# Kernel optimization log

Hardware: AMD Instinct MI355X
Metric: run time of the kernel (lower is better)

Reference implementation:

```python
import jax, jax.numpy as jnp
import numpy as np

B, T, S, O = 8, 60, 36, 1
H, E, PE = 4, 16, 16
AD, TA, OUT, L = 12, 10, 64, 2
PRUNE_KEEP_FROM = int(np.floor(S * S * 0.5))  # floor(S^2 * (1 - prune_rate))
EPS = 1e-5


def lrelu(v):
    return jax.nn.leaky_relu(v, 0.01)


def pos_encode(times):
    # standard sinusoidal PE on raw timestamps -> (B, T, PE)
    half = PE // 2
    div = jnp.exp(jnp.arange(half, dtype=jnp.float32) * (-jnp.log(10000.0) / half))
    ang = times[..., None] * div
    return jnp.stack([jnp.sin(ang), jnp.cos(ang)], axis=-1).reshape(times.shape + (PE,))


def pair_sim(adj):
    # sum_{i<j} ||a_i - a_j||^2 = B*sum_i||a_i||^2 - ||sum_i a_i||^2
    b = adj.shape[0]
    sq = jnp.sum(adj * adj)
    tot = jnp.sum(adj, axis=0)
    return (b * sq - jnp.sum(tot * tot)) / ((b - 1) ** 2) / (S * S)


def _forward(x, times, mask, bn_g, bn_b, obs_emb_w, attn_w, bidir_w, proj_W, proj_b,
             Wq, bq, Wk, bk, Ws, bs, lnt_g, lnt_b, Wse, bse, lns_g, lns_b):
    b = x.shape[0]
    # BatchNorm2d over timestep channels (training-mode batch stats)
    mu = x.mean(axis=(0, 2, 3), keepdims=True)
    var = x.var(axis=(0, 2, 3), keepdims=True)
    x = (x - mu) / jnp.sqrt(var + EPS) * bn_g[None, :, None, None] + bn_b[None, :, None, None]
    # per-sensor observation embedding: (B,T,S,O) x (S,O,E*H) -> (B,H,T,S,E)
    h = lrelu(jnp.einsum('btso,som->btsm', x, obs_emb_w))
    h = h.reshape(b, T, S, H, E).transpose(0, 3, 1, 2, 4)
    h = h * mask[:, None, :, :, None]
    pe = pos_encode(times)  # (B,T,PE)
    adj = jnp.ones((b, H, S, S), x.dtype)
    sim = pair_sim(adj)  # 0 for all-ones init, kept for faithfulness
    prune_msk = None
    for lay in range(L):
        hp = h @ proj_W.T + proj_b  # (B,H,T,S,AD+PE)
        cat = jnp.concatenate([
            jnp.broadcast_to(attn_w[lay][None, :, None], (b, H, T, S, AD)),
            jnp.broadcast_to(pe[:, None, :, None], (b, H, T, S, PE))], axis=-1)
        alpha = lrelu(jnp.einsum('bhtsd,bhtjd->bhtsj', hp, cat))  # (B,H,T,S,S)
        if lay:
            cnt = mask.sum(axis=1)[:, None, :, None]  # (B,1,S,1)
            adj = lrelu(adj * (alpha.sum(axis=2) / cnt))
            if prune_msk is None:
                flat = adj.reshape(b, H, S * S)
                ranks = jnp.argsort(jnp.argsort(flat, axis=-1), axis=-1)
                prune_msk = (ranks >= PRUNE_KEEP_FROM).astype(adj.dtype).reshape(b, H, S, S)
            adj = adj * prune_msk
            sim = sim + pair_sim(adj)
        bidir = lrelu(jnp.einsum('hsd,hjd->hsj', bidir_w[lay], bidir_w[lay]))  # (H,S,S)
        w = lrelu(bidir[None, :, None] * alpha * adj[:, :, None])  # (B,H,T,S,S)
        # broadcast message passing: (B,H,T,1,S,E) * (B,H,T,S,S,1) -> sum over source sensor
        h = lrelu(jnp.sum(lrelu(h[:, :, :, None, :, :] * w[..., None]), axis=4))
    pe_e = jnp.broadcast_to(pe[:, None, :, None], (b, H, T, S, PE))
    Hc = jnp.concatenate([h, pe_e], axis=-1).transpose(0, 1, 3, 2, 4)  # (B,H,S,T,E+PE)
    Q = Hc @ Wq.T + bq
    K = Hc @ Wk.T + bk
    beta = jnp.einsum('bhstd,bhsud->bhstu', Q, K)  # (B,H,S,T,T)
    beta = (beta @ Ws.T + bs)[..., 0]  # (B,H,S,T)
    m = beta.mean(axis=(-2, -1), keepdims=True)
    v = beta.var(axis=(-2, -1), keepdims=True)
    beta = (beta - m) / jnp.sqrt(v + EPS) * lnt_g + lnt_b
    out = lrelu(jnp.einsum('bhst,bhstd->bhsd', beta, Hc))
    out = lrelu(out @ Wse.T + bse)
    m2 = out.mean(axis=(-2, -1), keepdims=True)
    v2 = out.var(axis=(-2, -1), keepdims=True)
    out = (out - m2) / jnp.sqrt(v2 + EPS) * lns_g + lns_b
    out = out.transpose(0, 2, 1, 3).reshape(b, S, OUT)
    return out, sim


def setup_inputs():
    key = jax.random.key(0)
    ks = jax.random.split(key, 12)
    def rn(k, shape, scale=0.1):
        return jax.random.normal(k, shape, jnp.float32) * scale
    return {
        'x': jax.random.normal(ks[0], (B, T, S, O), jnp.float32),
        'times': jnp.tile(jnp.arange(T, dtype=jnp.float32), (B, 1)),
        'mask': jnp.ones((B, T, S), jnp.float32),
        'bn_g': jnp.ones((T,), jnp.float32),
        'bn_b': jnp.zeros((T,), jnp.float32),
        'obs_emb_w': rn(ks[1], (S, O, E * H)),
        'attn_w': rn(ks[2], (L, H, S, AD)),
        'bidir_w': rn(ks[3], (L, H, S, AD)),
        'proj_W': rn(ks[4], (AD + PE, E)),
        'proj_b': jnp.zeros((AD + PE,), jnp.float32),
        'Wq': rn(ks[5], (TA, E + PE)),
        'bq': jnp.zeros((TA,), jnp.float32),
        'Wk': rn(ks[6], (TA, E + PE)),
        'bk': jnp.zeros((TA,), jnp.float32),
        'Ws': rn(ks[7], (1, T)),
        'bs': jnp.zeros((1,), jnp.float32),
        'lnt_g': jnp.ones((S, T), jnp.float32),
        'lnt_b': jnp.zeros((S, T), jnp.float32),
        'Wse': rn(ks[8], (OUT // H, E + PE)),
        'bse': jnp.zeros((OUT // H,), jnp.float32),
        'lns_g': jnp.ones((S, OUT // H), jnp.float32),
        'lns_b': jnp.zeros((S, OUT // H), jnp.float32),
    }


def reference(x, times, mask, bn_g, bn_b, obs_emb_w, attn_w, bidir_w, proj_W, proj_b,
              Wq, bq, Wk, bk, Ws, bs, lnt_g, lnt_b, Wse, bse, lns_g, lns_b):
    return _forward(x, times, mask, bn_g, bn_b, obs_emb_w, attn_w, bidir_w, proj_W, proj_b,
                    Wq, bq, Wk, bk, Ws, bs, lnt_g, lnt_b, Wse, bse, lns_g, lns_b)
```

## Files before the change

kernel.cpp:

```cpp
#include <hip/hip_runtime.h>
#include <math.h>

#define Bc 8
#define Tc 60
#define Sc 36
#define Hc_ 4
#define Ec 16
#define PEc 16
#define ADc 12
#define TAc 10
#define OUTc 64
#define KEEP 648
#define EPSc 1e-5f
#define LOG1E4_8 1.15129254649702284f

#define WS_H2     18176
#define WS_H1     1124096
#define WS_ALPHA  2230016
#define WS_ADJ    4759808
#define WS_ADJP   4801280
#define WS_CNT    5050112
#define WS_PE     5050496
#define WS_BETA   WS_ALPHA
#define WS_PART   (WS_ALPHA + 69120)
#define WS_OUT2   (WS_ALPHA + 71424)
#define WS_PART2  (WS_ALPHA + 89856)

__device__ __forceinline__ float lrelu(float v){ return fmaxf(v, 0.01f*v); }

__global__ __launch_bounds__(256) void k_layer01(const float* __restrict__ x,
                          const float* __restrict__ times,
                          const float* __restrict__ mask,
                          const float* __restrict__ bn_g,
                          const float* __restrict__ bn_b,
                          const float* __restrict__ obs_w,
                          const float* __restrict__ attn,
                          const float* __restrict__ bidw,
                          const float* __restrict__ projW,
                          const float* __restrict__ projb,
                          float* __restrict__ ws){
    int idx = blockIdx.x;
    int t = idx % Tc; int bh = idx / Tc; int h = bh % Hc_; int b = bh / Hc_;
    int tid = threadIdx.x;
    __shared__ float sh_h[Sc*Ec];
    __shared__ float sh_h1[Sc*Ec];
    __shared__ float sh_pe[PEc];
    __shared__ float sh_at0T[ADc*Sc];
    __shared__ float sh_at1T[ADc*Sc];
    __shared__ float sh_bwT[ADc*Sc];
    __shared__ float sh_hp[Sc*28];
    __shared__ float sh_P[Sc];
    __shared__ float sh_w[Sc*Sc];
    __shared__ float sh_xn[Sc];
    __shared__ float sh_m[Sc];
    __shared__ float sred[8];
    float s0 = 0.f, s1 = 0.f;
    for (int i = tid; i < Bc*Sc; i += 256){
        float v = x[((i/Sc)*Tc + t)*Sc + (i%Sc)];
        s0 += v; s1 += v*v;
    }
    #pragma unroll
    for (int off = 32; off; off >>= 1){
        s0 += __shfl_down(s0, off, 64);
        s1 += __shfl_down(s1, off, 64);
    }
    if ((tid & 63) == 0){ sred[(tid>>6)*2] = s0; sred[(tid>>6)*2 + 1] = s1; }
    if (tid >= 64 && tid < 80){
        int q = tid - 64; int j = q >> 1;
        float ang = times[b*Tc + t] * expf(-(float)j * LOG1E4_8);
        float pv = (q & 1) ? cosf(ang) : sinf(ang);
        sh_pe[q] = pv;
        if (h == 0) ws[WS_PE + (b*Tc + t)*PEc + q] = pv;
    }
    for (int i = tid; i < ADc*Sc; i += 256){
        int d = i / Sc, j = i % Sc;
        sh_at0T[i] = attn[h*Sc*ADc + j*ADc + d];
        sh_at1T[i] = attn[(Hc_ + h)*Sc*ADc + j*ADc + d];
        sh_bwT[i]  = bidw[h*Sc*ADc + j*ADc + d];
    }
    __syncthreads();
    float mu  = (sred[0]+sred[2]+sred[4]+sred[6]) / (float)(Bc*Sc);
    float var = (sred[1]+sred[3]+sred[5]+sred[7]) / (float)(Bc*Sc) - mu*mu;
    if (tid < Sc){
        float xv = x[(b*Tc + t)*Sc + tid];
        sh_xn[tid] = (xv - mu) * rsqrtf(var + EPSc) * bn_g[t] + bn_b[t];
        sh_m[tid]  = mask[(b*Tc + t)*Sc + tid];
    }
    __syncthreads();
    for (int i = tid; i < Sc*Ec; i += 256){
        int s = i / Ec, e = i % Ec;
        sh_h[i] = lrelu(sh_xn[s]*obs_w[s*64 + h*Ec + e]) * sh_m[s];
    }
    __syncthreads();
    for (int i = tid; i < Sc*28; i += 256){
        int s = i / 28, d = i % 28;
        float acc = projb[d];
        const float* w = projW + d*Ec;
        const float* hh = sh_h + s*Ec;
        #pragma unroll
        for (int e = 0; e < Ec; e++) acc += hh[e]*w[e];
        sh_hp[i] = acc;
    }
    __syncthreads();
    if (tid < Sc){
        const float* hp = sh_hp + tid*28 + ADc;
        float p = 0.f;
        #pragma unroll
        for (int d = 0; d < PEc; d++) p += hp[d]*sh_pe[d];
        sh_P[tid] = p;
    }
    __syncthreads();
    for (int i = tid; i < Sc*Sc; i += 256){
        int s = i / Sc, j = i % Sc;
        const float* hp = sh_hp + s*28;
        float acc = sh_P[s];
        float bd = 0.f;
        #pragma unroll
        for (int d = 0; d < ADc; d++){
            acc += hp[d]*sh_at0T[d*Sc + j];
            bd  += sh_bwT[d*Sc + s]*sh_bwT[d*Sc + j];
        }
        sh_w[i] = lrelu(lrelu(bd)*lrelu(acc));
    }
    __syncthreads();
    float* h1g = ws + WS_H1 + (size_t)idx*Sc*Ec;
    for (int i = tid; i < Sc*Ec; i += 256){
        int s = i / Ec, e = i % Ec;
        float acc = 0.f;
        #pragma unroll 6
        for (int j = 0; j < Sc; j++) acc += lrelu(sh_h[j*Ec + e]*sh_w[s*Sc + j]);
        float v = lrelu(acc);
        sh_h1[i] = v;
        h1g[i] = v;
    }
    __syncthreads();
    for (int i = tid; i < Sc*28; i += 256){
        int s = i / 28, d = i % 28;
        float acc = projb[d];
        const float* w = projW + d*Ec;
        const float* hh = sh_h1 + s*Ec;
        #pragma unroll
        for (int e = 0; e < Ec; e++) acc += hh[e]*w[e];
        sh_hp[i] = acc;
    }
    __syncthreads();
    if (tid < Sc){
        const float* hp = sh_hp + tid*28 + ADc;
        float p = 0.f;
        #pragma unroll
        for (int d = 0; d < PEc; d++) p += hp[d]*sh_pe[d];
        sh_P[tid] = p;
    }
    __syncthreads();
    float* adst = ws + WS_ALPHA + (size_t)idx*Sc*Sc;
    for (int i = tid; i < Sc*Sc; i += 256){
        int s = i / Sc, j = i % Sc;
        const float* hp = sh_hp + s*28;
        float acc = sh_P[s];
        #pragma unroll
        for (int d = 0; d < ADc; d++) acc += hp[d]*sh_at1T[d*Sc + j];
        adst[i] = lrelu(acc);
    }
}

__global__ __launch_bounds__(256) void k_adjpart(const float* __restrict__ mask, float* __restrict__ ws){
    int bh = blockIdx.x / 6; int chunk = blockIdx.x % 6;
    int tid = threadIdx.x;
    const float4* a = (const float4*)(ws + WS_ALPHA + (size_t)bh*Tc*Sc*Sc) + (size_t)chunk*10*324;
    float4* p = (float4*)(ws + WS_ADJP + (size_t)blockIdx.x*Sc*Sc);
    for (int c = tid; c < 324; c += 256){
        float4 acc = make_float4(0.f, 0.f, 0.f, 0.f);
        #pragma unroll
        for (int tt = 0; tt < 10; tt++){
            float4 u = a[(size_t)tt*324 + c];
            acc.x += u.x; acc.y += u.y; acc.z += u.z; acc.w += u.w;
        }
        p[c] = acc;
    }
    if (chunk == 0 && (bh & 3) == 0 && tid < Sc){
        int b = bh >> 2;
        float c = 0.f;
        #pragma unroll 4
        for (int t = 0; t < Tc; t++) c += mask[(b*Tc + t)*Sc + tid];
        ws[WS_CNT + b*Sc + tid] = c;
    }
}

__global__ __launch_bounds__(256) void k_prune(float* __restrict__ ws){
    int bh = blockIdx.x / 24; int chunk = blockIdx.x % 24;
    int b = bh >> 2;
    int tid = threadIdx.x;
    __shared__ __align__(16) float sh_v[Sc*Sc];
    __shared__ float sh_cnt[Sc];
    const float4* p = (const float4*)(ws + WS_ADJP + (size_t)bh*6*Sc*Sc);
    for (int c = tid; c < 324; c += 256){
        float4 acc = make_float4(0.f, 0.f, 0.f, 0.f);
        #pragma unroll
        for (int q = 0; q < 6; q++){
            float4 u = p[(size_t)q*324 + c];
            acc.x += u.x; acc.y += u.y; acc.z += u.z; acc.w += u.w;
        }
        ((float4*)sh_v)[c] = acc;
    }
    if (tid < Sc) sh_cnt[tid] = ws[WS_CNT + b*Sc + tid];
    __syncthreads();
    for (int i = tid; i < Sc*Sc; i += 256){
        int s = i / Sc;
        sh_v[i] = lrelu(sh_v[i] / sh_cnt[s]);
    }
    __syncthreads();
    int r = tid >> 2; if (r > 53) r = 53;
    int part = tid & 3;
    int i = chunk*54 + r;
    float v = sh_v[i];
    const float4* v4 = (const float4*)sh_v + part*81;
    int a0 = part*324;
    int cnt = 0;
    #pragma unroll 9
    for (int j = 0; j < 81; j++){
        float4 u = v4[j];
        int k = a0 + j*4;
        cnt += (int)(u.x < v) + ((int)(u.x == v) & (int)(k   < i));
        cnt += (int)(u.y < v) + ((int)(u.y == v) & (int)(k+1 < i));
        cnt += (int)(u.z < v) + ((int)(u.z == v) & (int)(k+2 < i));
        cnt += (int)(u.w < v) + ((int)(u.w == v) & (int)(k+3 < i));
    }
    cnt += __shfl_down(cnt, 2, 4);
    cnt += __shfl_down(cnt, 1, 4);
    if (part == 0 && tid < 216)
        ws[WS_ADJ + bh*Sc*Sc + i] = (cnt >= KEEP) ? v : 0.f;
}

__global__ __launch_bounds__(256) void k_layer1mp(const float* __restrict__ bidw,
                                                  float* __restrict__ ws){
    int idx = blockIdx.x;
    int t = idx % Tc; int bh = idx / Tc; int h = bh % Hc_;
    int tid = threadIdx.x;
    __shared__ float sh_h[Sc*Ec];
    __shared__ float sh_w[Sc*Sc];
    __shared__ float sh_bwT[ADc*Sc];
    const float* hsrc = ws + WS_H1 + (size_t)idx*Sc*Ec;
    const float* al  = ws + WS_ALPHA + (size_t)idx*Sc*Sc;
    const float* adj = ws + WS_ADJ + bh*Sc*Sc;
    for (int i = tid; i < Sc*Ec; i += 256) sh_h[i] = hsrc[i];
    for (int i = tid; i < ADc*Sc; i += 256){
        int d = i / Sc, j = i % Sc;
        sh_bwT[i] = bidw[(Hc_ + h)*Sc*ADc + j*ADc + d];
    }
    __syncthreads();
    for (int i = tid; i < Sc*Sc; i += 256){
        int s = i / Sc, j = i % Sc;
        float bd = 0.f;
        #pragma unroll
        for (int d = 0; d < ADc; d++) bd += sh_bwT[d*Sc + s]*sh_bwT[d*Sc + j];
        sh_w[i] = lrelu(lrelu(bd)*al[i]*adj[i]);
    }
    __syncthreads();
    for (int i = tid; i < Sc*Ec; i += 256){
        int s = i / Ec, e = i % Ec;
        float acc = 0.f;
        #pragma unroll 6
        for (int j = 0; j < Sc; j++) acc += lrelu(sh_h[j*Ec + e]*sh_w[s*Sc + j]);
        ws[WS_H2 + ((size_t)(bh*Sc + s)*Tc + t)*Ec + e] = lrelu(acc);
    }
}

__global__ __launch_bounds__(64) void kF1(const float* __restrict__ Wq, const float* __restrict__ bq,
                   const float* __restrict__ Wk, const float* __restrict__ bk,
                   const float* __restrict__ Ws_, const float* __restrict__ bs_,
                   float* __restrict__ ws){
    int idx = blockIdx.x;
    int bh = idx / Sc; int b = bh / Hc_;
    int tid = threadIdx.x;
    __shared__ float sh_Hc[Tc*33];
    __shared__ float sh_K[Tc*11];
    __shared__ float sh_Wq[TAc*32];
    __shared__ float sh_WkT[32*TAc];
    __shared__ float sh_bq[TAc], sh_bk[TAc];
    __shared__ float sh_ws[Tc];
    __shared__ float sh_Kw[TAc];
    const float* h2c = ws + WS_H2 + (size_t)idx*Tc*Ec;
    for (int i4 = tid; i4 < Tc*4; i4 += 64){
        int t = i4 >> 2, c4 = i4 & 3;
        float4 u = *(const float4*)(h2c + i4*4);
        float* d = sh_Hc + t*33 + c4*4;
        d[0] = u.x; d[1] = u.y; d[2] = u.z; d[3] = u.w;
    }
    for (int i4 = tid; i4 < Tc*4; i4 += 64){
        int t = i4 >> 2, c4 = i4 & 3;
        float4 u = *(const float4*)(ws + WS_PE + (size_t)(b*Tc + t)*PEc + c4*4);
        float* d = sh_Hc + t*33 + Ec + c4*4;
        d[0] = u.x; d[1] = u.y; d[2] = u.z; d[3] = u.w;
    }
    for (int i = tid; i < TAc*32; i += 64){
        sh_Wq[i] = Wq[i];
        int d = i / 32, q = i % 32;
        sh_WkT[q*TAc + d] = Wk[i];
    }
    if (tid < TAc){ sh_bq[tid] = bq[tid]; sh_bk[tid] = bk[tid]; }
    if (tid < Tc) sh_ws[tid] = Ws_[tid];
    __syncthreads();
    for (int i = tid; i < Tc*TAc; i += 64){
        int t = i / TAc, d = i % TAc;
        const float* hc = sh_Hc + t*33;
        float acc = sh_bk[d];
        #pragma unroll
        for (int q = 0; q < 32; q++) acc += hc[q]*sh_WkT[q*TAc + d];
        sh_K[t*11 + d] = acc;
    }
    __syncthreads();
    if (tid < TAc){
        float acc = 0.f;
        #pragma unroll 4
        for (int t = 0; t < Tc; t++) acc += sh_K[t*11 + tid]*sh_ws[t];
        sh_Kw[tid] = acc;
    }
    __syncthreads();
    float bv = 0.f;
    float bsv = bs_[0];
    if (tid < Tc){
        const float* hc = sh_Hc + tid*33;
        float acc = bsv;
        #pragma unroll
        for (int d = 0; d < TAc; d++){
            const float* wq = sh_Wq + d*32;
            float qv = sh_bq[d];
            #pragma unroll
            for (int q = 0; q < 32; q++) qv += hc[q]*wq[q];
            acc += qv*sh_Kw[d];
        }
        bv = acc;
        ws[WS_BETA + idx*Tc + tid] = acc;
    }
    float p0 = (tid < Tc) ? bv : 0.f;
    float p1 = p0*bv;
    #pragma unroll
    for (int off = 32; off; off >>= 1){
        p0 += __shfl_down(p0, off, 64);
        p1 += __shfl_down(p1, off, 64);
    }
    if (tid == 0){
        ws[WS_PART + idx*2]     = p0;
        ws[WS_PART + idx*2 + 1] = p1;
    }
}

__global__ __launch_bounds__(64) void kF2(const float* __restrict__ lnt_g, const float* __restrict__ lnt_b,
                   const float* __restrict__ Wse, const float* __restrict__ bse,
                   float* __restrict__ ws){
    int idx = blockIdx.x;
    int s = idx % Sc; int bh = idx / Sc; int b = bh / Hc_;
    int tid = threadIdx.x;
    __shared__ float sh_Hc[Tc*33];
    __shared__ float sh_beta[Tc];
    __shared__ float sh_o1[32];
    __shared__ float sh_mi[2];
    float p0 = 0.f, p1 = 0.f;
    if (tid < Sc){
        p0 = ws[WS_PART + (bh*Sc + tid)*2];
        p1 = ws[WS_PART + (bh*Sc + tid)*2 + 1];
    }
    #pragma unroll
    for (int off = 32; off; off >>= 1){
        p0 += __shfl_down(p0, off, 64);
        p1 += __shfl_down(p1, off, 64);
    }
    if (tid == 0){
        float m = p0 / (float)(Sc*Tc);
        sh_mi[0] = m;
        sh_mi[1] = rsqrtf(p1 / (float)(Sc*Tc) - m*m + EPSc);
    }
    const float* h2c = ws + WS_H2 + (size_t)idx*Tc*Ec;
    for (int i4 = tid; i4 < Tc*4; i4 += 64){
        int t = i4 >> 2, c4 = i4 & 3;
        float4 u = *(const float4*)(h2c + i4*4);
        float* d = sh_Hc + t*33 + c4*4;
        d[0] = u.x; d[1] = u.y; d[2] = u.z; d[3] = u.w;
    }
    for (int i4 = tid; i4 < Tc*4; i4 += 64){
        int t = i4 >> 2, c4 = i4 & 3;
        float4 u = *(const float4*)(ws + WS_PE + (size_t)(b*Tc + t)*PEc + c4*4);
        float* d = sh_Hc + t*33 + Ec + c4*4;
        d[0] = u.x; d[1] = u.y; d[2] = u.z; d[3] = u.w;
    }
    __syncthreads();
    float m = sh_mi[0], inv = sh_mi[1];
    if (tid < Tc){
        float bvv = ws[WS_BETA + idx*Tc + tid];
        sh_beta[tid] = (bvv - m)*inv*lnt_g[s*Tc + tid] + lnt_b[s*Tc + tid];
    }
    __syncthreads();
    if (tid < 32){
        float acc = 0.f;
        #pragma unroll 4
        for (int t = 0; t < Tc; t++) acc += sh_beta[t]*sh_Hc[t*33 + tid];
        sh_o1[tid] = lrelu(acc);
    }
    __syncthreads();
    float v = 0.f;
    if (tid < 16){
        float acc = bse[tid];
        const float* w = Wse + tid*32;
        #pragma unroll
        for (int d = 0; d < 32; d++) acc += sh_o1[d]*w[d];
        v = lrelu(acc);
        ws[WS_OUT2 + idx*16 + tid] = v;
    }
    float q0 = v, q1 = v*v;
    #pragma unroll
    for (int off = 32; off; off >>= 1){
        q0 += __shfl_down(q0, off, 64);
        q1 += __shfl_down(q1, off, 64);
    }
    if (tid == 0){
        ws[WS_PART2 + idx*2]     = q0;
        ws[WS_PART2 + idx*2 + 1] = q1;
    }
}

__global__ __launch_bounds__(256) void kF3s(const float* __restrict__ lns_g, const float* __restrict__ lns_b,
                    const float* __restrict__ ws, float* __restrict__ out){
    int tid = threadIdx.x;
    if (blockIdx.x == 32){
        float sq = 0.f, t2 = 0.f;
        for (int i = tid; i < Hc_*Sc*Sc; i += 256){
            float tot = 0.f;
            #pragma unroll
            for (int b = 0; b < Bc; b++){
                float v = ws[WS_ADJ + b*Hc_*Sc*Sc + i];
                sq += v*v; tot += v;
            }
            t2 += tot*tot;
        }
        __shared__ float r0[256], r1[256];
        r0[tid] = sq; r1[tid] = t2; __syncthreads();
        for (int off = 128; off; off >>= 1){
            if (tid < off){ r0[tid] += r0[tid+off]; r1[tid] += r1[tid+off]; }
            __syncthreads();
        }
        if (tid == 0)
            out[Bc*Sc*OUTc] = ((float)Bc*r0[0] - r1[0]) / 49.f / 1296.f;
        return;
    }
    int bh = blockIdx.x; int h = bh % Hc_; int b = bh / Hc_;
    __shared__ float sh_mi[2];
    if (tid < 64){
        float p0 = 0.f, p1 = 0.f;
        if (tid < Sc){
            p0 = ws[WS_PART2 + (bh*Sc + tid)*2];
            p1 = ws[WS_PART2 + (bh*Sc + tid)*2 + 1];
        }
        #pragma unroll
        for (int off = 32; off; off >>= 1){
            p0 += __shfl_down(p0, off, 64);
            p1 += __shfl_down(p1, off, 64);
        }
        if (tid == 0){
            float m = p0 / (float)(Sc*16);
            sh_mi[0] = m;
            sh_mi[1] = rsqrtf(p1 / (float)(Sc*16) - m*m + EPSc);
        }
    }
    __syncthreads();
    float m2 = sh_mi[0], inv2 = sh_mi[1];
    for (int i = tid; i < Sc*16; i += 256){
        int s = i / 16, k = i % 16;
        float v = ws[WS_OUT2 + bh*Sc*16 + i];
        out[(b*Sc + s)*OUTc + h*16 + k] = (v - m2)*inv2*lns_g[i] + lns_b[i];
    }
}

extern "C" void kernel_launch(void* const* d_in, const int* in_sizes, int n_in,
                              void* d_out, int out_size, void* d_ws, size_t ws_size,
                              hipStream_t stream){
    const float* x     = (const float*)d_in[0];
    const float* times = (const float*)d_in[1];
    const float* mask  = (const float*)d_in[2];
    const float* bn_g  = (const float*)d_in[3];
    const float* bn_b  = (const float*)d_in[4];
    const float* obs   = (const float*)d_in[5];
    const float* attn  = (const float*)d_in[6];
    const float* bidw  = (const float*)d_in[7];
    const float* projW = (const float*)d_in[8];
    const float* projb = (const float*)d_in[9];
    const float* Wq    = (const float*)d_in[10];
    const float* bq    = (const float*)d_in[11];
    const float* Wk    = (const float*)d_in[12];
    const float* bk    = (const float*)d_in[13];
    const float* Ws_   = (const float*)d_in[14];
    const float* bs_   = (const float*)d_in[15];
    const float* lnt_g = (const float*)d_in[16];
    const float* lnt_b = (const float*)d_in[17];
    const float* Wse   = (const float*)d_in[18];
    const float* bse   = (const float*)d_in[19];
    const float* lns_g = (const float*)d_in[20];
    const float* lns_b = (const float*)d_in[21];
    float* ws  = (float*)d_ws;
    float* out = (float*)d_out;

    k_layer01<<<Bc*Hc_*Tc, 256, 0, stream>>>(x, times, mask, bn_g, bn_b, obs, attn, bidw, projW, projb, ws);
    k_adjpart<<<Bc*Hc_*6, 256, 0, stream>>>(mask, ws);
    k_prune<<<Bc*Hc_*24, 256, 0, stream>>>(ws);
    k_layer1mp<<<Bc*Hc_*Tc, 256, 0, stream>>>(bidw, ws);
    kF1<<<Bc*Hc_*Sc, 64, 0, stream>>>(Wq, bq, Wk, bk, Ws_, bs_, ws);
    kF2<<<Bc*Hc_*Sc, 64, 0, stream>>>(lnt_g, lnt_b, Wse, bse, ws);
    kF3s<<<Bc*Hc_ + 1, 256, 0, stream>>>(lns_g, lns_b, ws, out);
}
```

Before: 201.6 us.

## Fuse reductions into producer kernels via last-block atomic counters

Removes the k_adjpart and kF3s launches. k_layer01 and kF2 now use per-(b,h) atomic completion counters, and the last-arriving block does the time-sum of alpha or the final layernorm/output write. The mask count moves into k_layer01, and the pair-similarity scalar moves to an extra block of k_layer1mp, which also resets the second counter. This cuts launch overhead and intermediate traffic. The cost is a memset launch, fence/atomic overhead, and a serial tail where one block sums 60 alpha slices.

```diff
diff --git a/kernel.cpp b/kernel.cpp
--- a/kernel.cpp
+++ b/kernel.cpp
@@ -21,6 +21,8 @@
 #define WS_ADJP   4801280
 #define WS_CNT    5050112
 #define WS_PE     5050496
+#define WS_DONE1  5058176
+#define WS_DONE2  5058208
 #define WS_BETA   WS_ALPHA
 #define WS_PART   (WS_ALPHA + 69120)
 #define WS_OUT2   (WS_ALPHA + 71424)
@@ -54,6 +56,7 @@
     __shared__ float sh_xn[Sc];
     __shared__ float sh_m[Sc];
     __shared__ float sred[8];
+    __shared__ int sh_last;
     float s0 = 0.f, s1 = 0.f;
     for (int i = tid; i < Bc*Sc; i += 256){
         float v = x[((i/Sc)*Tc + t)*Sc + (i%Sc)];
@@ -71,6 +74,13 @@
         float pv = (q & 1) ? cosf(ang) : sinf(ang);
         sh_pe[q] = pv;
         if (h == 0) ws[WS_PE + (b*Tc + t)*PEc + q] = pv;
+    }
+    if (t == 0 && h == 0 && tid >= 128 && tid < 128 + Sc){
+        int ss = tid - 128;
+        float c = 0.f;
+        #pragma unroll 4
+        for (int tt = 0; tt < Tc; tt++) c += mask[(b*Tc + tt)*Sc + ss];
+        ws[WS_CNT + b*Sc + ss] = c;
     }
     for (int i = tid; i < ADc*Sc; i += 256){
         int d = i / Sc, j = i % Sc;
@@ -161,28 +171,32 @@
         for (int d = 0; d < ADc; d++) acc += hp[d]*sh_at1T[d*Sc + j];
         adst[i] = lrelu(acc);
     }
-}
-
-__global__ __launch_bounds__(256) void k_adjpart(const float* __restrict__ mask, float* __restrict__ ws){
-    int bh = blockIdx.x / 6; int chunk = blockIdx.x % 6;
-    int tid = threadIdx.x;
-    const float4* a = (const float4*)(ws + WS_ALPHA + (size_t)bh*Tc*Sc*Sc) + (size_t)chunk*10*324;
-    float4* p = (float4*)(ws + WS_ADJP + (size_t)blockIdx.x*Sc*Sc);
-    for (int c = tid; c < 324; c += 256){
-        float4 acc = make_float4(0.f, 0.f, 0.f, 0.f);
-        #pragma unroll
-        for (int tt = 0; tt < 10; tt++){
-            float4 u = a[(size_t)tt*324 + c];
-            acc.x += u.x; acc.y += u.y; acc.z += u.z; acc.w += u.w;
-        }
-        p[c] = acc;
-    }
-    if (chunk == 0 && (bh & 3) == 0 && tid < Sc){
-        int b = bh >> 2;
-        float c = 0.f;
-        #pragma unroll 4
-        for (int t = 0; t < Tc; t++) c += mask[(b*Tc + t)*Sc + tid];
-        ws[WS_CNT + b*Sc + tid] = c;
+    __syncthreads();
+    if (tid == 0){
+        __threadfence();
+        unsigned old = atomicAdd((unsigned*)(ws + WS_DONE1) + bh, 1u);
+        sh_last = (old == Tc - 1);
+    }
+    __syncthreads();
+    if (sh_last){
+        if (tid == 0) __threadfence();
+        __syncthreads();
+        const float4* a = (const float4*)(ws + WS_ALPHA + (size_t)bh*Tc*Sc*Sc);
+        float4* p = (float4*)(ws + WS_ADJP + (size_t)bh*Sc*Sc);
+        for (int c = tid; c < 324; c += 256){
+            float4 acc = make_float4(0.f, 0.f, 0.f, 0.f);
+            #pragma unroll
+            for (int q = 0; q < 6; q++){
+                float4 pq = make_float4(0.f, 0.f, 0.f, 0.f);
+                #pragma unroll
+                for (int tt = 0; tt < 10; tt++){
+                    float4 u = a[(size_t)(q*10 + tt)*324 + c];
+                    pq.x += u.x; pq.y += u.y; pq.z += u.z; pq.w += u.w;
+                }
+                acc.x += pq.x; acc.y += pq.y; acc.z += pq.z; acc.w += pq.w;
+            }
+            p[c] = acc;
+        }
     }
 }
 
@@ -192,16 +206,8 @@
     int tid = threadIdx.x;
     __shared__ __align__(16) float sh_v[Sc*Sc];
     __shared__ float sh_cnt[Sc];
-    const float4* p = (const float4*)(ws + WS_ADJP + (size_t)bh*6*Sc*Sc);
-    for (int c = tid; c < 324; c += 256){
-        float4 acc = make_float4(0.f, 0.f, 0.f, 0.f);
-        #pragma unroll
-        for (int q = 0; q < 6; q++){
-            float4 u = p[(size_t)q*324 + c];
-            acc.x += u.x; acc.y += u.y; acc.z += u.z; acc.w += u.w;
-        }
-        ((float4*)sh_v)[c] = acc;
-    }
+    const float4* p = (const float4*)(ws + WS_ADJP + (size_t)bh*Sc*Sc);
+    for (int c = tid; c < 324; c += 256) ((float4*)sh_v)[c] = p[c];
     if (tid < Sc) sh_cnt[tid] = ws[WS_CNT + b*Sc + tid];
     __syncthreads();
     for (int i = tid; i < Sc*Sc; i += 256){
@@ -232,13 +238,36 @@
 }
 
 __global__ __launch_bounds__(256) void k_layer1mp(const float* __restrict__ bidw,
-                                                  float* __restrict__ ws){
-    int idx = blockIdx.x;
-    int t = idx % Tc; int bh = idx / Tc; int h = bh % Hc_;
+                                                  float* __restrict__ ws,
+                                                  float* __restrict__ out){
     int tid = threadIdx.x;
     __shared__ float sh_h[Sc*Ec];
     __shared__ float sh_w[Sc*Sc];
     __shared__ float sh_bwT[ADc*Sc];
+    if (blockIdx.x == Bc*Hc_*Tc){
+        if (tid < 32) ((int*)(ws + WS_DONE2))[tid] = 0;
+        float sq = 0.f, t2 = 0.f;
+        for (int i = tid; i < Hc_*Sc*Sc; i += 256){
+            float tot = 0.f;
+            #pragma unroll
+            for (int b = 0; b < Bc; b++){
+                float v = ws[WS_ADJ + b*Hc_*Sc*Sc + i];
+                sq += v*v; tot += v;
+            }
+            t2 += tot*tot;
+        }
+        float* r0 = sh_w; float* r1 = sh_w + 256;
+        r0[tid] = sq; r1[tid] = t2; __syncthreads();
+        for (int off = 128; off; off >>= 1){
+            if (tid < off){ r0[tid] += r0[tid+off]; r1[tid] += r1[tid+off]; }
+            __syncthreads();
+        }
+        if (tid == 0)
+            out[Bc*Sc*OUTc] = ((float)Bc*r0[0] - r1[0]) / 49.f / 1296.f;
+        return;
+    }
+    int idx = blockIdx.x;
+    int t = idx % Tc; int bh = idx / Tc; int h = bh % Hc_;
     const float* hsrc = ws + WS_H1 + (size_t)idx*Sc*Ec;
     const float* al  = ws + WS_ALPHA + (size_t)idx*Sc*Sc;
     const float* adj = ws + WS_ADJ + bh*Sc*Sc;
@@ -347,14 +376,16 @@
 
 __global__ __launch_bounds__(64) void kF2(const float* __restrict__ lnt_g, const float* __restrict__ lnt_b,
                    const float* __restrict__ Wse, const float* __restrict__ bse,
-                   float* __restrict__ ws){
+                   const float* __restrict__ lns_g, const float* __restrict__ lns_b,
+                   float* __restrict__ ws, float* __restrict__ out){
     int idx = blockIdx.x;
-    int s = idx % Sc; int bh = idx / Sc; int b = bh / Hc_;
+    int s = idx % Sc; int bh = idx / Sc; int b = bh / Hc_; int h = bh % Hc_;
     int tid = threadIdx.x;
     __shared__ float sh_Hc[Tc*33];
     __shared__ float sh_beta[Tc];
     __shared__ float sh_o1[32];
     __shared__ float sh_mi[2];
+    __shared__ int sh_last;
     float p0 = 0.f, p1 = 0.f;
     if (tid < Sc){
         p0 = ws[WS_PART + (bh*Sc + tid)*2];
@@ -416,57 +447,37 @@
         ws[WS_PART2 + idx*2]     = q0;
         ws[WS_PART2 + idx*2 + 1] = q1;
     }
-}
-
-__global__ __launch_bounds__(256) void kF3s(const float* __restrict__ lns_g, const float* __restrict__ lns_b,
-                    const float* __restrict__ ws, float* __restrict__ out){
-    int tid = threadIdx.x;
-    if (blockIdx.x == 32){
-        float sq = 0.f, t2 = 0.f;
-        for (int i = tid; i < Hc_*Sc*Sc; i += 256){
-            float tot = 0.f;
-            #pragma unroll
-            for (int b = 0; b < Bc; b++){
-                float v = ws[WS_ADJ + b*Hc_*Sc*Sc + i];
-                sq += v*v; tot += v;
-            }
-            t2 += tot*tot;
-        }
-        __shared__ float r0[256], r1[256];
-        r0[tid] = sq; r1[tid] = t2; __syncthreads();
-        for (int off = 128; off; off >>= 1){
-            if (tid < off){ r0[tid] += r0[tid+off]; r1[tid] += r1[tid+off]; }
-            __syncthreads();
-        }
-        if (tid == 0)
-            out[Bc*Sc*OUTc] = ((float)Bc*r0[0] - r1[0]) / 49.f / 1296.f;
-        return;
-    }
-    int bh = blockIdx.x; int h = bh % Hc_; int b = bh / Hc_;
-    __shared__ float sh_mi[2];
-    if (tid < 64){
-        float p0 = 0.f, p1 = 0.f;
+    if (tid == 0){
+        __threadfence();
+        unsigned old = atomicAdd((unsigned*)(ws + WS_DONE2) + bh, 1u);
+        sh_last = (old == Sc - 1);
+    }
+    __syncthreads();
+    if (sh_last){
+        if (tid == 0) __threadfence();
+        __syncthreads();
+        float r0 = 0.f, r1 = 0.f;
         if (tid < Sc){
-            p0 = ws[WS_PART2 + (bh*Sc + tid)*2];
-            p1 = ws[WS_PART2 + (bh*Sc + tid)*2 + 1];
+            r0 = ws[WS_PART2 + (bh*Sc + tid)*2];
+            r1 = ws[WS_PART2 + (bh*Sc + tid)*2 + 1];
         }
         #pragma unroll
         for (int off = 32; off; off >>= 1){
-            p0 += __shfl_down(p0, off, 64);
-            p1 += __shfl_down(p1, off, 64);
+            r0 += __shfl_down(r0, off, 64);
+            r1 += __shfl_down(r1, off, 64);
         }
         if (tid == 0){
-            float m = p0 / (float)(Sc*16);
-            sh_mi[0] = m;
-            sh_mi[1] = rsqrtf(p1 / (float)(Sc*16) - m*m + EPSc);
-        }
-    }
-    __syncthreads();
-    float m2 = sh_mi[0], inv2 = sh_mi[1];
-    for (int i = tid; i < Sc*16; i += 256){
-        int s = i / 16, k = i % 16;
-        float v = ws[WS_OUT2 + bh*Sc*16 + i];
-        out[(b*Sc + s)*OUTc + h*16 + k] = (v - m2)*inv2*lns_g[i] + lns_b[i];
+            float mm = r0 / (float)(Sc*16);
+            sh_mi[0] = mm;
+            sh_mi[1] = rsqrtf(r1 / (float)(Sc*16) - mm*mm + EPSc);
+        }
+        __syncthreads();
+        float m2 = sh_mi[0], inv2 = sh_mi[1];
+        for (int i = tid; i < Sc*16; i += 64){
+            int ss = i / 16, k = i % 16;
+            float vv = ws[WS_OUT2 + bh*Sc*16 + i];
+            out[(b*Sc + ss)*OUTc + h*16 + k] = (vv - m2)*inv2*lns_g[i] + lns_b[i];
+        }
     }
 }
 
@@ -498,11 +509,11 @@
     float* ws  = (float*)d_ws;
     float* out = (float*)d_out;
 
+    hipMemsetAsync(ws + WS_DONE1, 0, 32*sizeof(unsigned), stream);
+
     k_layer01<<<Bc*Hc_*Tc, 256, 0, stream>>>(x, times, mask, bn_g, bn_b, obs, attn, bidw, projW, projb, ws);
-    k_adjpart<<<Bc*Hc_*6, 256, 0, stream>>>(mask, ws);
     k_prune<<<Bc*Hc_*24, 256, 0, stream>>>(ws);
-    k_layer1mp<<<Bc*Hc_*Tc, 256, 0, stream>>>(bidw, ws);
+    k_layer1mp<<<Bc*Hc_*Tc + 1, 256, 0, stream>>>(bidw, ws, out);
     kF1<<<Bc*Hc_*Sc, 64, 0, stream>>>(Wq, bq, Wk, bk, Ws_, bs_, ws);
-    kF2<<<Bc*Hc_*Sc, 64, 0, stream>>>(lnt_g, lnt_b, Wse, bse, ws);
-    kF3s<<<Bc*Hc_ + 1, 256, 0, stream>>>(lns_g, lns_b, ws, out);
+    kF2<<<Bc*Hc_*Sc, 64, 0, stream>>>(lnt_g, lnt_b, Wse, bse, lns_g, lns_b, ws, out);
 }
```

Result: slower. 277.1 us (+37.5%).
